# Optimization experiments

Measured on AMD Instinct MI355X. Metric: run time of the kernel, lower is better.

## Reference

```python
import jax, jax.numpy as jnp
import numpy as np

N = 1048576
D = 64
BATCH = 1024


def setup_inputs() -> dict:
    key = jax.random.key(0)
    k1, k2, k3, k4 = jax.random.split(key, 4)
    x = jax.random.normal(k1, (N, D), dtype=jnp.float32)
    A = jax.random.normal(k2, (D, D), dtype=jnp.float32)
    b = jax.random.normal(k3, (D,), dtype=jnp.float32)
    theta = jax.random.normal(k4, (D,), dtype=jnp.float32)
    return {"x": x, "A": A, "b": b, "theta": theta, "K": 1024}


def reference(x, A, b, theta, K):
    # z = x @ A + b  -> [N, D]
    z = jnp.dot(x, A) + b[None, :]
    # log p(x|z): -0.5 * ||x - z||^2 per row  -> [N]
    log_xGz = -0.5 * jnp.sum((x - z) ** 2, axis=1)
    # log p(z): -0.5 * ||z - theta||^2 per row (vectorizes the original loop)
    log_z = -0.5 * jnp.sum((z - theta[None, :]) ** 2, axis=1)
    log_weight = (log_xGz + log_z)[: BATCH * K].reshape(BATCH, K)
    # IWAE: softmax weights are detached (stop_gradient)
    weight = jax.lax.stop_gradient(jax.nn.softmax(log_weight, axis=1))
    ELBO = -jnp.mean(jnp.sum(weight * log_weight, axis=1))
    return ELBO
```

## Files before the change

kernel.cpp:

```cpp
#include <hip/hip_runtime.h>
#include <hip/hip_bf16.h>


typedef __attribute__((ext_vector_type(8))) short short8;
typedef __attribute__((ext_vector_type(4))) float floatx4;

#define WS_QT 0
#define WS_V  8192
#define WS_C  8448
#define WS_R  8704

__device__ __forceinline__ short bf16r(float f) {
  __hip_bfloat16 h = __float2bfloat16(f);
  short r; __builtin_memcpy(&r, &h, 2); return r;
}

__device__ __forceinline__ short8 cvt_bf16x8(float4 a, float4 b) {
  short8 r;
  r[0]=bf16r(a.x); r[1]=bf16r(a.y); r[2]=bf16r(a.z); r[3]=bf16r(a.w);
  r[4]=bf16r(b.x); r[5]=bf16r(b.y); r[6]=bf16r(b.z); r[7]=bf16r(b.w);
  return r;
}

__global__ void prep_kernel(const float* __restrict__ A, const float* __restrict__ b,
                            const float* __restrict__ th, unsigned short* __restrict__ Qt,
                            float* __restrict__ v, float* __restrict__ cws) {
  const int k = blockIdx.x, d = threadIdx.x;
  float qs = 0.f;
  for (int j = 0; j < 64; ++j) qs = fmaf(A[k*64+j], A[d*64+j], qs);
  float Qkd = (k == d ? 1.f : 0.f) + 2.f*qs - A[k*64+d] - A[d*64+k];
  __hip_bfloat16 h = __float2bfloat16(Qkd);
  unsigned short u; __builtin_memcpy(&u, &h, 2);
  Qt[d*64 + k] = u;
  if (k == 0) {
    float s = -2.f*b[d];
    for (int j = 0; j < 64; ++j) s = fmaf(A[d*64+j], 4.f*b[j] - 2.f*th[j], s);
    v[d] = s;
    if (d == 0) {
      float cc = 0.f;
      for (int j = 0; j < 64; ++j) cc += 2.f*b[j]*b[j] - 2.f*b[j]*th[j] + th[j]*th[j];
      *cws = cc;
    }
  }
}

__global__ __launch_bounds__(256) void main_kernel(
    const float* __restrict__ x, const unsigned short* __restrict__ Qt,
    const float* __restrict__ v, const float* __restrict__ cptr,
    float* __restrict__ rbuf) {
  __shared__ __align__(16) float xlds[4][16*68];
  __shared__ __align__(16) float lws[1024];
  __shared__ float wredA[4], wredB[4], wredC[4];

  const int tid = threadIdx.x;
  const int w = tid >> 6, l = tid & 63, q = l >> 4, s = l & 15;
  const int n0 = blockIdx.x << 10;

  short8 bfrag[2][4];
  #pragma unroll
  for (int ks = 0; ks < 2; ++ks)
    #pragma unroll
    for (int tt = 0; tt < 4; ++tt)
      bfrag[ks][tt] = *(const short8*)(Qt + (tt*16 + s)*64 + ks*32 + q*8);

  float vreg[4];
  #pragma unroll
  for (int tt = 0; tt < 4; ++tt) vreg[tt] = v[tt*16 + s];
  const float cc = *cptr;

  float* xw = &xlds[w][s*68 + q*8];

  for (int t = 0; t < 16; ++t) {
    const int row0 = (w*16 + t)*16;
    const float* xp = x + ((size_t)(n0 + row0 + s))*64 + q*8;
    float4 xa = *(const float4*)(xp);
    float4 xb = *(const float4*)(xp + 4);
    float4 xc = *(const float4*)(xp + 32);
    float4 xd = *(const float4*)(xp + 36);

    short8 af0 = cvt_bf16x8(xa, xb);
    short8 af1 = cvt_bf16x8(xc, xd);

    floatx4 acc[4];
    #pragma unroll
    for (int tt = 0; tt < 4; ++tt) {
      floatx4 z4 = {0.f, 0.f, 0.f, 0.f};
      acc[tt] = __builtin_amdgcn_mfma_f32_16x16x32_bf16(af0, bfrag[0][tt], z4, 0, 0, 0);
      acc[tt] = __builtin_amdgcn_mfma_f32_16x16x32_bf16(af1, bfrag[1][tt], acc[tt], 0, 0, 0);
    }

    *(float4*)(xw)      = xa;
    *(float4*)(xw + 4)  = xb;
    *(float4*)(xw + 32) = xc;
    *(float4*)(xw + 36) = xd;

    float pl[4] = {0.f, 0.f, 0.f, 0.f};
    #pragma unroll
    for (int tt = 0; tt < 4; ++tt) {
      const float* xr = &xlds[w][(q*4)*68 + tt*16 + s];
      #pragma unroll
      for (int r = 0; r < 4; ++r)
        pl[r] = fmaf(acc[tt][r] + vreg[tt], xr[r*68], pl[r]);
    }
    #pragma unroll
    for (int r = 0; r < 4; ++r) {
      float p = pl[r];
      p += __shfl_xor(p, 1, 64);
      p += __shfl_xor(p, 2, 64);
      p += __shfl_xor(p, 4, 64);
      p += __shfl_xor(p, 8, 64);
      pl[r] = -0.5f * (p + cc);
    }
    if (s == 0) {
      float4 st = make_float4(pl[0], pl[1], pl[2], pl[3]);
      *(float4*)&lws[row0 + q*4] = st;
    }
  }

  __syncthreads();
  float4 mv = ((const float4*)lws)[tid];
  float mx = fmaxf(fmaxf(mv.x, mv.y), fmaxf(mv.z, mv.w));
  #pragma unroll
  for (int m = 1; m < 64; m <<= 1) mx = fmaxf(mx, __shfl_xor(mx, m, 64));
  if (l == 0) wredA[w] = mx;
  __syncthreads();
  const float bmax = fmaxf(fmaxf(wredA[0], wredA[1]), fmaxf(wredA[2], wredA[3]));

  float s1 = 0.f, s2 = 0.f, e;
  e = __expf(mv.x - bmax); s1 += e; s2 = fmaf(e, mv.x, s2);
  e = __expf(mv.y - bmax); s1 += e; s2 = fmaf(e, mv.y, s2);
  e = __expf(mv.z - bmax); s1 += e; s2 = fmaf(e, mv.z, s2);
  e = __expf(mv.w - bmax); s1 += e; s2 = fmaf(e, mv.w, s2);
  #pragma unroll
  for (int m = 1; m < 64; m <<= 1) {
    s1 += __shfl_xor(s1, m, 64);
    s2 += __shfl_xor(s2, m, 64);
  }
  if (l == 0) { wredB[w] = s1; wredC[w] = s2; }
  __syncthreads();
  if (tid == 0) {
    float S1 = wredB[0] + wredB[1] + wredB[2] + wredB[3];
    float S2 = wredC[0] + wredC[1] + wredC[2] + wredC[3];
    rbuf[blockIdx.x] = S2 / S1;
  }
}

__global__ void finish_kernel(const float* __restrict__ rbuf, float* __restrict__ out) {
  __shared__ float wsum[4];
  const int tid = threadIdx.x;
  float4 vv = ((const float4*)rbuf)[tid];
  float s = vv.x + vv.y + vv.z + vv.w;
  #pragma unroll
  for (int m = 1; m < 64; m <<= 1) s += __shfl_xor(s, m, 64);
  if ((tid & 63) == 0) wsum[tid >> 6] = s;
  __syncthreads();
  if (tid == 0) out[0] = -(wsum[0] + wsum[1] + wsum[2] + wsum[3]) * (1.0f / 1024.0f);
}

extern "C" void kernel_launch(void* const* d_in, const int* in_sizes, int n_in,
                              void* d_out, int out_size, void* d_ws, size_t ws_size,
                              hipStream_t stream) {
  const float* x  = (const float*)d_in[0];
  const float* A  = (const float*)d_in[1];
  const float* b  = (const float*)d_in[2];
  const float* th = (const float*)d_in[3];
  char* ws = (char*)d_ws;
  unsigned short* Qt = (unsigned short*)(ws + WS_QT);
  float* v    = (float*)(ws + WS_V);
  float* cws  = (float*)(ws + WS_C);
  float* rbuf = (float*)(ws + WS_R);
  float* out  = (float*)d_out;

  prep_kernel<<<64, 64, 0, stream>>>(A, b, th, Qt, v, cws);
  main_kernel<<<1024, 256, 0, stream>>>(x, Qt, v, cws, rbuf);
  finish_kernel<<<1, 256, 0, stream>>>(rbuf, out);
}
```

Baseline: 374.6 us.

## Compute residuals directly via 64x128 MFMA and prefetch next x tile

The quadratic-form formulation (x^T Q x + v·x + c) is replaced by computing both residuals x - z and z - theta directly through one 64x128 matrix U with the bias folded into the accumulator init, then summing squares. This removes the LDS staging of x, the cross-lane products, and the A^T A precompute. It doubles MFMA count per tile. It also software-prefetches the next tile's x loads into registers to overlap global loads with compute. Register pressure grows from 16 B-fragments and the prefetch buffers.

```diff
diff --git a/kernel.cpp b/kernel.cpp
--- a/kernel.cpp
+++ b/kernel.cpp
@@ -5,10 +5,9 @@
 typedef __attribute__((ext_vector_type(8))) short short8;
 typedef __attribute__((ext_vector_type(4))) float floatx4;
 
-#define WS_QT 0
-#define WS_V  8192
-#define WS_C  8448
-#define WS_R  8704
+#define WS_UT 0
+#define WS_CV 16384
+#define WS_R  17920
 
 __device__ __forceinline__ short bf16r(float f) {
   __hip_bfloat16 h = __float2bfloat16(f);
@@ -23,32 +22,22 @@
 }
 
 __global__ void prep_kernel(const float* __restrict__ A, const float* __restrict__ b,
-                            const float* __restrict__ th, unsigned short* __restrict__ Qt,
-                            float* __restrict__ v, float* __restrict__ cws) {
-  const int k = blockIdx.x, d = threadIdx.x;
-  float qs = 0.f;
-  for (int j = 0; j < 64; ++j) qs = fmaf(A[k*64+j], A[d*64+j], qs);
-  float Qkd = (k == d ? 1.f : 0.f) + 2.f*qs - A[k*64+d] - A[d*64+k];
-  __hip_bfloat16 h = __float2bfloat16(Qkd);
-  unsigned short u; __builtin_memcpy(&u, &h, 2);
-  Qt[d*64 + k] = u;
-  if (k == 0) {
-    float s = -2.f*b[d];
-    for (int j = 0; j < 64; ++j) s = fmaf(A[d*64+j], 4.f*b[j] - 2.f*th[j], s);
-    v[d] = s;
-    if (d == 0) {
-      float cc = 0.f;
-      for (int j = 0; j < 64; ++j) cc += 2.f*b[j]*b[j] - 2.f*b[j]*th[j] + th[j]*th[j];
-      *cws = cc;
-    }
-  }
+                            const float* __restrict__ th,
+                            unsigned short* __restrict__ Ut, float* __restrict__ cvec) {
+  const int i = blockIdx.x * 256 + threadIdx.x;
+  const int k = i >> 7, n = i & 127;
+  float u;
+  if (n < 64) u = (k == n ? 1.f : 0.f) - A[k*64 + n];
+  else        u = A[k*64 + (n - 64)];
+  __hip_bfloat16 h = __float2bfloat16(u);
+  unsigned short us; __builtin_memcpy(&us, &h, 2);
+  Ut[n*64 + k] = us;
+  if (i < 128) cvec[i] = (i < 64) ? -b[i] : (b[i - 64] - th[i - 64]);
 }
 
 __global__ __launch_bounds__(256) void main_kernel(
-    const float* __restrict__ x, const unsigned short* __restrict__ Qt,
-    const float* __restrict__ v, const float* __restrict__ cptr,
-    float* __restrict__ rbuf) {
-  __shared__ __align__(16) float xlds[4][16*68];
+    const float* __restrict__ x, const unsigned short* __restrict__ Ut,
+    const float* __restrict__ cvec, float* __restrict__ rbuf) {
   __shared__ __align__(16) float lws[1024];
   __shared__ float wredA[4], wredB[4], wredC[4];
 
@@ -56,65 +45,61 @@
   const int w = tid >> 6, l = tid & 63, q = l >> 4, s = l & 15;
   const int n0 = blockIdx.x << 10;
 
-  short8 bfrag[2][4];
+  short8 bfrag[2][8];
   #pragma unroll
   for (int ks = 0; ks < 2; ++ks)
     #pragma unroll
-    for (int tt = 0; tt < 4; ++tt)
-      bfrag[ks][tt] = *(const short8*)(Qt + (tt*16 + s)*64 + ks*32 + q*8);
+    for (int u = 0; u < 8; ++u)
+      bfrag[ks][u] = *(const short8*)(Ut + (u*16 + s)*64 + ks*32 + q*8);
 
-  float vreg[4];
+  float cv[8];
   #pragma unroll
-  for (int tt = 0; tt < 4; ++tt) vreg[tt] = v[tt*16 + s];
-  const float cc = *cptr;
+  for (int u = 0; u < 8; ++u) cv[u] = cvec[u*16 + s];
 
-  float* xw = &xlds[w][s*68 + q*8];
+  const float* base = x + ((size_t)(n0 + w*256 + s))*64 + q*8;
 
+  float4 c0 = *(const float4*)(base);
+  float4 c1 = *(const float4*)(base + 4);
+  float4 c2 = *(const float4*)(base + 32);
+  float4 c3 = *(const float4*)(base + 36);
+
+  #pragma unroll 2
   for (int t = 0; t < 16; ++t) {
-    const int row0 = (w*16 + t)*16;
-    const float* xp = x + ((size_t)(n0 + row0 + s))*64 + q*8;
-    float4 xa = *(const float4*)(xp);
-    float4 xb = *(const float4*)(xp + 4);
-    float4 xc = *(const float4*)(xp + 32);
-    float4 xd = *(const float4*)(xp + 36);
+    const float* pn = base + (size_t)((t < 15 ? t + 1 : 15)) * 1024;
+    float4 p0 = *(const float4*)(pn);
+    float4 p1 = *(const float4*)(pn + 4);
+    float4 p2 = *(const float4*)(pn + 32);
+    float4 p3 = *(const float4*)(pn + 36);
 
-    short8 af0 = cvt_bf16x8(xa, xb);
-    short8 af1 = cvt_bf16x8(xc, xd);
+    short8 af0 = cvt_bf16x8(c0, c1);
+    short8 af1 = cvt_bf16x8(c2, c3);
 
-    floatx4 acc[4];
+    float sl[4] = {0.f, 0.f, 0.f, 0.f};
     #pragma unroll
-    for (int tt = 0; tt < 4; ++tt) {
-      floatx4 z4 = {0.f, 0.f, 0.f, 0.f};
-      acc[tt] = __builtin_amdgcn_mfma_f32_16x16x32_bf16(af0, bfrag[0][tt], z4, 0, 0, 0);
-      acc[tt] = __builtin_amdgcn_mfma_f32_16x16x32_bf16(af1, bfrag[1][tt], acc[tt], 0, 0, 0);
+    for (int u = 0; u < 8; ++u) {
+      floatx4 acc = {cv[u], cv[u], cv[u], cv[u]};
+      acc = __builtin_amdgcn_mfma_f32_16x16x32_bf16(af0, bfrag[0][u], acc, 0, 0, 0);
+      acc = __builtin_amdgcn_mfma_f32_16x16x32_bf16(af1, bfrag[1][u], acc, 0, 0, 0);
+      #pragma unroll
+      for (int r = 0; r < 4; ++r) sl[r] = fmaf(acc[r], acc[r], sl[r]);
     }
 
-    *(float4*)(xw)      = xa;
-    *(float4*)(xw + 4)  = xb;
-    *(float4*)(xw + 32) = xc;
-    *(float4*)(xw + 36) = xd;
-
-    float pl[4] = {0.f, 0.f, 0.f, 0.f};
-    #pragma unroll
-    for (int tt = 0; tt < 4; ++tt) {
-      const float* xr = &xlds[w][(q*4)*68 + tt*16 + s];
-      #pragma unroll
-      for (int r = 0; r < 4; ++r)
-        pl[r] = fmaf(acc[tt][r] + vreg[tt], xr[r*68], pl[r]);
-    }
     #pragma unroll
     for (int r = 0; r < 4; ++r) {
-      float p = pl[r];
+      float p = sl[r];
       p += __shfl_xor(p, 1, 64);
       p += __shfl_xor(p, 2, 64);
       p += __shfl_xor(p, 4, 64);
       p += __shfl_xor(p, 8, 64);
-      pl[r] = -0.5f * (p + cc);
+      sl[r] = -0.5f * p;
     }
     if (s == 0) {
-      float4 st = make_float4(pl[0], pl[1], pl[2], pl[3]);
+      const int row0 = w*256 + t*16;
+      float4 st = make_float4(sl[0], sl[1], sl[2], sl[3]);
       *(float4*)&lws[row0 + q*4] = st;
     }
+
+    c0 = p0; c1 = p1; c2 = p2; c3 = p3;
   }
 
   __syncthreads();
@@ -165,13 +150,12 @@
   const float* b  = (const float*)d_in[2];
   const float* th = (const float*)d_in[3];
   char* ws = (char*)d_ws;
-  unsigned short* Qt = (unsigned short*)(ws + WS_QT);
-  float* v    = (float*)(ws + WS_V);
-  float* cws  = (float*)(ws + WS_C);
+  unsigned short* Ut = (unsigned short*)(ws + WS_UT);
+  float* cvec = (float*)(ws + WS_CV);
   float* rbuf = (float*)(ws + WS_R);
   float* out  = (float*)d_out;
 
-  prep_kernel<<<64, 64, 0, stream>>>(A, b, th, Qt, v, cws);
-  main_kernel<<<1024, 256, 0, stream>>>(x, Qt, v, cws, rbuf);
+  prep_kernel<<<32, 256, 0, stream>>>(A, b, th, Ut, cvec);
+  main_kernel<<<1024, 256, 0, stream>>>(x, Ut, cvec, rbuf);
   finish_kernel<<<1, 256, 0, stream>>>(rbuf, out);
 }
```

New measurement: 371.4 us. About the same (-0.9%).
